# Performance work log

Measured on AMD Instinct MI355X. Metric: run time of the kernel, lower is better.

The kernel has to match this reference:

```python
import jax, jax.numpy as jnp
import numpy as np

L = 4       # num_fourier_layers
W = 256     # width
NF = 256    # num_freq (no_low_freq)
B = 2       # batch size
N = 16384   # num_nodes per graph
E = 524288  # total edges (avg degree 16)
D_IN = 3    # darcy input features


def lin(x, w, b):
    # torch nn.Linear convention: w is (out, in)
    return x @ w.T + b


def layernorm(x, s, b):
    m = x.mean(-1, keepdims=True)
    v = x.var(-1, keepdims=True)
    return (x - m) / jnp.sqrt(v + 1e-5) * s + b


def setup_inputs() -> dict:
    key = jax.random.key(0)
    ks = jax.random.split(key, 16)
    s = lambda i, shape, sc=0.05: sc * jax.random.normal(ks[i], shape, jnp.float32)
    inp = {
        "x": jax.random.normal(ks[0], (B * N, D_IN), jnp.float32),
        "U": jax.random.normal(ks[1], (B, N, NF), jnp.float32) / np.float32(np.sqrt(N)),
        "edge_index": jax.random.randint(ks[2], (2, E), 0, B * N),
        "edge_weight": jax.random.uniform(ks[3], (E,), jnp.float32),
        "lif_embed": jax.random.normal(ks[4], (B * N, 16), jnp.float32),
        "p_w": s(5, (W, D_IN)), "p_b": jnp.zeros((W,), jnp.float32),
        # scale = 1/(in*out) * rand, per GraphFourierLayer
        "four_w": (1.0 / (W * W)) * jax.random.uniform(ks[6], (L, W, W, NF), jnp.float32),
        "w_w": s(7, (L, W, W)), "w_b": jnp.zeros((L, W), jnp.float32),
        "ln_s": jnp.ones((L, W), jnp.float32), "ln_b": jnp.zeros((L, W), jnp.float32),
        "lin_w": s(8, (L, W, W)), "lin_b": jnp.zeros((L, W), jnp.float32),
        "ew_w": s(9, (L, 16, 1)), "ew_b": jnp.zeros((L, 16), jnp.float32),
        "g1_w": s(10, (L, 3, 48)), "g1_b": jnp.zeros((L, 3), jnp.float32),
        "g2_w": s(11, (L, 1, 3)), "g2_b": jnp.zeros((L, 1), jnp.float32),
        "proj_w": s(12, (W, 2 * W)), "proj_b": jnp.zeros((W,), jnp.float32),
        "q1_w": s(13, (128, W)), "q1_b": jnp.zeros((128,), jnp.float32),
        "q2_w": s(14, (1, 128)), "q2_b": jnp.zeros((1,), jnp.float32),
    }
    return inp


def reference(x, U, edge_index, edge_weight, lif_embed,
              p_w, p_b, four_w, w_w, w_b, ln_s, ln_b,
              lin_w, lin_b, ew_w, ew_b, g1_w, g1_b, g2_w, g2_b,
              proj_w, proj_b, q1_w, q1_b, q2_w, q2_b):
    src = edge_index[0]  # edge_index_j (source)
    dst = edge_index[1]  # edge_index_i (target, aggr='add')
    h = lin(x, p_w, p_b)  # [B*N, W]

    for l in range(L):
        # --- GraphFourierLayer: batched spectral transform ---
        h3 = h.reshape(B, N, W)
        x_ft = jnp.einsum('bnf,bnw->bfw', U, h3)          # U^T x  -> [B, NF, W]
        out_ft = jnp.einsum('bfi,iof->bfo', x_ft, four_w[l])
        x1 = jnp.einsum('bnf,bfw->bnw', U, out_ft).reshape(B * N, W)
        xf = jax.nn.gelu(x1 + lin(h, w_w[l], w_b[l]), approximate=False)
        xf = layernorm(xf, ln_s[l], ln_b[l])

        # --- FrigateConv: gather -> edge MLP gate -> scatter-add -> L2 normalize ---
        xs = lin(h, lin_w[l], lin_b[l])
        ew = lin(edge_weight[:, None], ew_w[l], ew_b[l])  # [E, 16]
        gin = jnp.concatenate([ew, lif_embed[dst], lif_embed[src]], axis=1)  # [E, 48]
        g = jax.nn.sigmoid(lin(jax.nn.relu(lin(gin, g1_w[l], g1_b[l])), g2_w[l], g2_b[l]))
        msg = xs[src] * g                                  # [E, W]
        agg = jax.ops.segment_sum(msg, dst, num_segments=B * N)
        nrm = jnp.maximum(jnp.linalg.norm(agg, axis=-1, keepdims=True), 1e-12)
        xs = agg / nrm

        h = lin(jnp.concatenate([xf, xs], axis=1), proj_w, proj_b)

    out = lin(jax.nn.relu(lin(h, q1_w, q1_b)), q2_w, q2_b)  # q: MLP(W,1,128)
    return out
```

## Files before the change

### kernel.cpp

```cpp
#include <hip/hip_runtime.h>
#include <hip/hip_bf16.h>

#define B_ 2
#define N_ 16384
#define BN 32768
#define W_ 256
#define NF_ 256
#define E_ 524288
#define L_ 4
#define KS_ 32

typedef __attribute__((ext_vector_type(8))) short bf16x8;
typedef __attribute__((ext_vector_type(4))) float f32x4;

__device__ __forceinline__ unsigned short f2b(float x) {
    __hip_bfloat16 h = __float2bfloat16(x);
    return *reinterpret_cast<unsigned short*>(&h);
}
__device__ __forceinline__ float b2f(unsigned short u) {
    union { unsigned int i; float f; } c; c.i = ((unsigned int)u) << 16; return c.f;
}
__device__ __forceinline__ float geluf(float x) {
    return 0.5f * x * (1.0f + erff(x * 0.70710678118654752440f));
}

template<bool DUAL, int OUTM, bool BIAS>
__global__ __launch_bounds__(256) void k_mfma_nt(
    const unsigned short* __restrict__ A1, int lda1, long A1o, long A1i,
    const unsigned short* __restrict__ B1, int ldb1, long B1o, long B1i, int K1,
    const unsigned short* __restrict__ A2, int lda2, long A2o,
    const unsigned short* __restrict__ B2, int ldb2, long B2o, int K2,
    void* __restrict__ Cv, int ldc, long Co, long Ci,
    const float* __restrict__ bias, int zdiv)
{
    __shared__ unsigned short lds[16384];
    const int t = threadIdx.x;
    const int wid = t >> 6, lane = t & 63;
    const int wr = wid >> 1, wc = wid & 1;
    const int m0 = blockIdx.y * 128, n0 = blockIdx.x * 128;
    const int z = blockIdx.z;
    const int zo = z / zdiv, zi = z - zo * zdiv;
    A1 += zo * A1o + zi * A1i;
    B1 += zo * B1o + zi * B1i;
    if (DUAL) { A2 += zo * A2o; B2 += zo * B2o; }

    const int srow  = t >> 3;
    const int sgran = (t & 7) ^ (srow & 7);
    const int rlo   = lane & 15;
    const int hi    = lane >> 4;

    f32x4 acc[4][4] = {};

    const int nph = DUAL ? 2 : 1;
    for (int ph = 0; ph < nph; ++ph) {
        const unsigned short* A  = (DUAL && ph) ? A2 : A1;
        const unsigned short* Bp = (DUAL && ph) ? B2 : B1;
        const int lda = (DUAL && ph) ? lda2 : lda1;
        const int ldb = (DUAL && ph) ? ldb2 : ldb1;
        const int K   = (DUAL && ph) ? K2 : K1;
        for (int k0 = 0; k0 < K; k0 += 64) {
            __syncthreads();
            #pragma unroll
            for (int j = 0; j < 4; ++j) {
                const unsigned short* ga = A + (long)(m0 + j*32 + srow) * lda + k0 + sgran*8;
                __builtin_amdgcn_global_load_lds(
                    (const __attribute__((address_space(1))) void*)ga,
                    (__attribute__((address_space(3))) void*)&lds[(j*4 + wid) * 512],
                    16, 0, 0);
            }
            #pragma unroll
            for (int j = 0; j < 4; ++j) {
                const unsigned short* gb = Bp + (long)(n0 + j*32 + srow) * ldb + k0 + sgran*8;
                __builtin_amdgcn_global_load_lds(
                    (const __attribute__((address_space(1))) void*)gb,
                    (__attribute__((address_space(3))) void*)&lds[8192 + (j*4 + wid) * 512],
                    16, 0, 0);
            }
            __syncthreads();
            #pragma unroll
            for (int kk = 0; kk < 2; ++kk) {
                const int g8 = (((kk*4 + hi) ^ (lane & 7)) << 3);
                bf16x8 a[4], b[4];
                #pragma unroll
                for (int fm = 0; fm < 4; ++fm)
                    a[fm] = *(const bf16x8*)&lds[(wr*64 + fm*16 + rlo)*64 + g8];
                #pragma unroll
                for (int fn = 0; fn < 4; ++fn)
                    b[fn] = *(const bf16x8*)&lds[8192 + (wc*64 + fn*16 + rlo)*64 + g8];
                #pragma unroll
                for (int fm = 0; fm < 4; ++fm)
                    #pragma unroll
                    for (int fn = 0; fn < 4; ++fn)
                        acc[fm][fn] = __builtin_amdgcn_mfma_f32_16x16x32_bf16(
                            a[fm], b[fn], acc[fm][fn], 0, 0, 0);
            }
        }
    }

    const int mb = m0 + wr*64, nb = n0 + wc*64;
    if (OUTM == 1) {
        unsigned short* C = (unsigned short*)Cv + zo * Co + zi * Ci;
        #pragma unroll
        for (int fn = 0; fn < 4; ++fn) {
            const int n = nb + fn*16 + rlo;
            const float bv = BIAS ? bias[n] : 0.f;
            #pragma unroll
            for (int fm = 0; fm < 4; ++fm)
                #pragma unroll
                for (int r = 0; r < 4; ++r) {
                    const int m = mb + fm*16 + hi*4 + r;
                    C[(long)m*ldc + n] = f2b(acc[fm][fn][r] + bv);
                }
        }
    } else {
        float* C = (float*)Cv + zo * Co + zi * Ci;
        #pragma unroll
        for (int fn = 0; fn < 4; ++fn) {
            const int n = nb + fn*16 + rlo;
            const float bv = BIAS ? bias[n] : 0.f;
            #pragma unroll
            for (int fm = 0; fm < 4; ++fm)
                #pragma unroll
                for (int r = 0; r < 4; ++r) {
                    const int m = mb + fm*16 + hi*4 + r;
                    C[(long)m*ldc + n] = acc[fm][fn][r] + bv;
                }
        }
    }
}

__global__ __launch_bounds__(256) void k_cvt(const float* __restrict__ s, unsigned short* __restrict__ d) {
    long i = (long)(blockIdx.x * 256 + threadIdx.x) * 4;
    float4 v = *(const float4*)&s[i];
    ushort4 u = {f2b(v.x), f2b(v.y), f2b(v.z), f2b(v.w)};
    *(ushort4*)&d[i] = u;
}

__global__ __launch_bounds__(256) void k_cvtT(
    const float* __restrict__ src, unsigned short* __restrict__ dT, unsigned short* __restrict__ dL)
{
    const int b = blockIdx.z;
    src += (long)b * N_ * NF_; dT += (long)b * N_ * NF_; dL += (long)b * N_ * NF_;
    const int r0 = blockIdx.y * 64, c0 = blockIdx.x * 64;
    __shared__ unsigned short tile[64][72];
    const int t = threadIdx.x, lr = t >> 4, lc4 = (t & 15) * 4;
    #pragma unroll
    for (int p = 0; p < 4; ++p) {
        int r = p*16 + lr;
        float4 v = *(const float4*)&src[(long)(r0+r)*NF_ + c0 + lc4];
        ushort4 u = {f2b(v.x), f2b(v.y), f2b(v.z), f2b(v.w)};
        *(ushort4*)&dL[(long)(r0+r)*NF_ + c0 + lc4] = u;
        tile[r][lc4+0]=u.x; tile[r][lc4+1]=u.y; tile[r][lc4+2]=u.z; tile[r][lc4+3]=u.w;
    }
    __syncthreads();
    #pragma unroll
    for (int p = 0; p < 4; ++p) {
        int c = p*16 + lr;
        ushort4 u = {tile[lc4+0][c], tile[lc4+1][c], tile[lc4+2][c], tile[lc4+3][c]};
        *(ushort4*)&dT[(long)(c0+c)*N_ + r0 + lc4] = u;
    }
}

__global__ __launch_bounds__(256) void k_T_b2b(
    const unsigned short* __restrict__ src, unsigned short* __restrict__ dst)
{
    const int b = blockIdx.z;
    src += (long)b * N_ * W_; dst += (long)b * N_ * W_;
    const int r0 = blockIdx.y * 64, c0 = blockIdx.x * 64;
    __shared__ unsigned short tile[64][72];
    const int t = threadIdx.x, lr = t >> 4, lc4 = (t & 15) * 4;
    #pragma unroll
    for (int p = 0; p < 4; ++p) {
        int r = p*16 + lr;
        ushort4 v = *(const ushort4*)&src[(long)(r0+r)*W_ + c0 + lc4];
        tile[r][lc4+0]=v.x; tile[r][lc4+1]=v.y; tile[r][lc4+2]=v.z; tile[r][lc4+3]=v.w;
    }
    __syncthreads();
    #pragma unroll
    for (int p = 0; p < 4; ++p) {
        int c = p*16 + lr;
        ushort4 u = {tile[lc4+0][c], tile[lc4+1][c], tile[lc4+2][c], tile[lc4+3][c]};
        *(ushort4*)&dst[(long)(c0+c)*N_ + r0 + lc4] = u;
    }
}

__global__ __launch_bounds__(256) void k_in_proj(
    const float* __restrict__ x, const float* __restrict__ pw,
    const float* __restrict__ pb, unsigned short* __restrict__ h)
{
    int idx = blockIdx.x * 256 + threadIdx.x;
    int node = idx >> 8, w = idx & 255;
    float x0 = x[node*3+0], x1 = x[node*3+1], x2 = x[node*3+2];
    h[idx] = f2b(fmaf(x0, pw[w*3+0], fmaf(x1, pw[w*3+1], fmaf(x2, pw[w*3+2], pb[w]))));
}

__global__ __launch_bounds__(256) void k_reduce_ks(
    const float* __restrict__ part, float* __restrict__ outp)
{
    int idx = blockIdx.x * 256 + threadIdx.x;
    int b = idx >> 16, rem = idx & 65535;
    const float* p = part + (long)b * KS_ * 65536 + rem;
    float s = 0.f;
    #pragma unroll
    for (int k = 0; k < KS_; ++k) s += p[(long)k * 65536];
    outp[idx] = s;
}

__global__ __launch_bounds__(256) void k_fourier_mul(
    const float* __restrict__ fw, const float* __restrict__ xftT,
    unsigned short* __restrict__ oftT)
{
    const int o = blockIdx.x, f = threadIdx.x;
    const float* fwp = fw + (long)o * NF_ + f;
    float a0 = 0.f, a1 = 0.f;
    #pragma unroll 8
    for (int i = 0; i < W_; ++i) {
        float w = fwp[(long)i * W_ * NF_];
        a0 = fmaf(xftT[i*NF_ + f], w, a0);
        a1 = fmaf(xftT[65536 + i*NF_ + f], w, a1);
    }
    oftT[o*NF_ + f] = f2b(a0);
    oftT[65536 + o*NF_ + f] = f2b(a1);
}

__global__ __launch_bounds__(256) void k_gelu_ln(
    const float* __restrict__ xf, unsigned short* __restrict__ out,
    const float* __restrict__ wb, const float* __restrict__ lns, const float* __restrict__ lnb)
{
    const int node = blockIdx.x * 4 + (threadIdx.x >> 6);
    const int lane = threadIdx.x & 63;
    float4 v = *(const float4*)(xf + (long)node*W_ + lane*4);
    float4 bb = *(const float4*)(wb + lane*4);
    float e0 = geluf(v.x+bb.x), e1 = geluf(v.y+bb.y);
    float e2 = geluf(v.z+bb.z), e3 = geluf(v.w+bb.w);
    float s  = e0+e1+e2+e3;
    float s2 = e0*e0+e1*e1+e2*e2+e3*e3;
    #pragma unroll
    for (int o = 32; o; o >>= 1) { s += __shfl_xor(s, o); s2 += __shfl_xor(s2, o); }
    float mean = s * (1.0f/W_);
    float var  = s2 * (1.0f/W_) - mean*mean;
    float inv = rsqrtf(var + 1e-5f);
    float4 sc = *(const float4*)(lns + lane*4);
    float4 bi = *(const float4*)(lnb + lane*4);
    ushort4 o4;
    o4.x = f2b((e0-mean)*inv*sc.x + bi.x);
    o4.y = f2b((e1-mean)*inv*sc.y + bi.y);
    o4.z = f2b((e2-mean)*inv*sc.z + bi.z);
    o4.w = f2b((e3-mean)*inv*sc.w + bi.w);
    *(ushort4*)(out + (long)node*W_ + lane*4) = o4;
}

__global__ __launch_bounds__(256) void k_hist(const int* __restrict__ ei, int* __restrict__ count) {
    int e = blockIdx.x * 256 + threadIdx.x;
    atomicAdd(&count[ei[E_ + e]], 1);
}
__global__ __launch_bounds__(256) void k_scan(const int* __restrict__ count, int* __restrict__ offsets) {
    __shared__ int sums[256];
    const int t = threadIdx.x;
    const int base = t * 128;
    int s = 0;
    for (int i = 0; i < 128; ++i) s += count[base + i];
    sums[t] = s;
    __syncthreads();
    for (int off = 1; off < 256; off <<= 1) {
        int v = (t >= off) ? sums[t - off] : 0;
        __syncthreads();
        sums[t] += v;
        __syncthreads();
    }
    int run = (t == 0) ? 0 : sums[t - 1];
    for (int i = 0; i < 128; ++i) { offsets[base + i] = run; run += count[base + i]; }
    if (t == 255) offsets[BN] = run;
}
__global__ __launch_bounds__(256) void k_place(
    const int* __restrict__ ei, const float* __restrict__ ewt,
    const int* __restrict__ offsets, int* __restrict__ cursor,
    int* __restrict__ srcp, float* __restrict__ ewt_p)
{
    int e = blockIdx.x * 256 + threadIdx.x;
    int dst = ei[E_ + e];
    int pos = offsets[dst] + atomicAdd(&cursor[dst], 1);
    srcp[pos] = ei[e];
    ewt_p[pos] = ewt[e];
}

__global__ __launch_bounds__(256) void k_gate_agg(
    const int* __restrict__ offsets, const int* __restrict__ srcp,
    const float* __restrict__ ewt_p, const float* __restrict__ lif,
    const float* __restrict__ eww, const float* __restrict__ ewb,
    const float* __restrict__ g1w, const float* __restrict__ g1b,
    const float* __restrict__ g2w, const float* __restrict__ g2b,
    const unsigned short* __restrict__ xs, unsigned short* __restrict__ out)
{
    const int node = blockIdx.x * 4 + (threadIdx.x >> 6);
    const int lane = threadIdx.x & 63;
    const int beg = offsets[node], end = offsets[node + 1];
    float lifd[16];
    #pragma unroll
    for (int j = 0; j < 16; ++j) lifd[j] = lif[node*16 + j];
    float a0=0.f, a1=0.f, a2=0.f, a3=0.f;
    for (int c0 = beg; c0 < end; c0 += 64) {
        const int p = c0 + lane;
        float gate = 0.f; int src = 0;
        if (p < end) {
            src = srcp[p];
            const float wv = ewt_p[p];
            float t0 = g1b[0], t1 = g1b[1], t2 = g1b[2];
            #pragma unroll
            for (int j = 0; j < 16; ++j) {
                const float e0 = fmaf(wv, eww[j], ewb[j]);
                const float l1 = lifd[j];
                const float l2 = lif[src*16 + j];
                t0 = fmaf(g1w[j], e0, t0);
                t0 = fmaf(g1w[16 + j], l1, t0);
                t0 = fmaf(g1w[32 + j], l2, t0);
                t1 = fmaf(g1w[48 + j], e0, t1);
                t1 = fmaf(g1w[64 + j], l1, t1);
                t1 = fmaf(g1w[80 + j], l2, t1);
                t2 = fmaf(g1w[96 + j], e0, t2);
                t2 = fmaf(g1w[112 + j], l1, t2);
                t2 = fmaf(g1w[128 + j], l2, t2);
            }
            float z = g2b[0];
            z = fmaf(g2w[0], fmaxf(t0, 0.f), z);
            z = fmaf(g2w[1], fmaxf(t1, 0.f), z);
            z = fmaf(g2w[2], fmaxf(t2, 0.f), z);
            gate = 1.f / (1.f + __expf(-z));
        }
        const int m = min(64, end - c0);
        for (int j = 0; j < m; ++j) {
            const float gv = __shfl(gate, j);
            const int   s  = __shfl(src, j);
            ushort4 v = *(const ushort4*)&xs[(long)s * W_ + lane * 4];
            a0 = fmaf(b2f(v.x), gv, a0);
            a1 = fmaf(b2f(v.y), gv, a1);
            a2 = fmaf(b2f(v.z), gv, a2);
            a3 = fmaf(b2f(v.w), gv, a3);
        }
    }
    float s = a0*a0 + a1*a1 + a2*a2 + a3*a3;
    #pragma unroll
    for (int o = 32; o; o >>= 1) s += __shfl_xor(s, o);
    float inv = 1.f / fmaxf(sqrtf(s), 1e-12f);
    ushort4 r = {f2b(a0*inv), f2b(a1*inv), f2b(a2*inv), f2b(a3*inv)};
    *(ushort4*)(out + (long)node * W_ + lane * 4) = r;
}

__global__ __launch_bounds__(256) void k_q2(
    const float* __restrict__ q1o, const float* __restrict__ q2w,
    const float* __restrict__ q2b, float* __restrict__ out)
{
    int node = blockIdx.x * 4 + (threadIdx.x >> 6);
    int lane = threadIdx.x & 63;
    float a = fmaxf(q1o[(long)node*128 + lane], 0.f) * q2w[lane]
            + fmaxf(q1o[(long)node*128 + 64 + lane], 0.f) * q2w[64 + lane];
    #pragma unroll
    for (int o = 32; o; o >>= 1) a += __shfl_xor(a, o);
    if (lane == 0) out[node] = a + q2b[0];
}

extern "C" void kernel_launch(void* const* d_in, const int* in_sizes, int n_in,
                              void* d_out, int out_size, void* d_ws, size_t ws_size,
                              hipStream_t stream)
{
    const float* x      = (const float*)d_in[0];
    const float* U      = (const float*)d_in[1];
    const int*   ei     = (const int*)  d_in[2];
    const float* ewt    = (const float*)d_in[3];
    const float* lif    = (const float*)d_in[4];
    const float* p_w    = (const float*)d_in[5];
    const float* p_b    = (const float*)d_in[6];
    const float* four_w = (const float*)d_in[7];
    const float* w_w    = (const float*)d_in[8];
    const float* w_b    = (const float*)d_in[9];
    const float* ln_s   = (const float*)d_in[10];
    const float* ln_b   = (const float*)d_in[11];
    const float* lin_w  = (const float*)d_in[12];
    const float* lin_b  = (const float*)d_in[13];
    const float* ew_w   = (const float*)d_in[14];
    const float* ew_b   = (const float*)d_in[15];
    const float* g1_w   = (const float*)d_in[16];
    const float* g1_b   = (const float*)d_in[17];
    const float* g2_w   = (const float*)d_in[18];
    const float* g2_b   = (const float*)d_in[19];
    const float* proj_w = (const float*)d_in[20];
    const float* proj_b = (const float*)d_in[21];
    const float* q1_w   = (const float*)d_in[22];
    const float* q1_b   = (const float*)d_in[23];
    const float* q2_w   = (const float*)d_in[24];
    const float* q2_b   = (const float*)d_in[25];

    char* wsb = (char*)d_ws;
    size_t off = 0;
    auto alloc = [&](size_t bytes) -> void* {
        void* p = wsb + off; off += (bytes + 255) & ~(size_t)255; return p;
    };
    float* xf        = (float*)alloc((size_t)BN * W_ * 4);
    float* xft_part  = (float*)alloc((size_t)B_ * KS_ * 65536 * 4);
    float* xftT      = (float*)alloc((size_t)B_ * 65536 * 4);
    unsigned short* h_bf   = (unsigned short*)alloc((size_t)BN * W_ * 2);
    unsigned short* hT_bf  = (unsigned short*)alloc((size_t)BN * W_ * 2);
    unsigned short* U_bf   = (unsigned short*)alloc((size_t)BN * NF_ * 2);
    unsigned short* UT_bf  = (unsigned short*)alloc((size_t)BN * NF_ * 2);
    unsigned short* xf_bf  = (unsigned short*)alloc((size_t)BN * W_ * 2);
    unsigned short* xs_bf  = (unsigned short*)alloc((size_t)BN * W_ * 2);
    unsigned short* xsn_bf = (unsigned short*)alloc((size_t)BN * W_ * 2);
    unsigned short* oftT_bf= (unsigned short*)alloc((size_t)B_ * 65536 * 2);
    unsigned short* wwb    = (unsigned short*)alloc((size_t)L_ * W_ * W_ * 2);
    unsigned short* linwb  = (unsigned short*)alloc((size_t)L_ * W_ * W_ * 2);
    unsigned short* projwb = (unsigned short*)alloc((size_t)W_ * 2 * W_ * 2);
    unsigned short* q1wb   = (unsigned short*)alloc((size_t)128 * W_ * 2);
    int*   srcp    = (int*)alloc((size_t)E_ * 4);
    float* ewt_p   = (float*)alloc((size_t)E_ * 4);
    int*   count   = (int*)alloc((size_t)BN * 4);
    int*   cursor  = (int*)alloc((size_t)BN * 4);
    int*   offsets = (int*)alloc((size_t)(BN + 1) * 4);

    hipMemsetAsync(count, 0, (size_t)2 * BN * 4, stream);
    k_hist<<<E_/256, 256, 0, stream>>>(ei, count);
    k_scan<<<1, 256, 0, stream>>>(count, offsets);
    k_place<<<E_/256, 256, 0, stream>>>(ei, ewt, offsets, cursor, srcp, ewt_p);

    k_cvt<<<(L_*W_*W_)/1024, 256, 0, stream>>>(w_w, wwb);
    k_cvt<<<(L_*W_*W_)/1024, 256, 0, stream>>>(lin_w, linwb);
    k_cvt<<<(W_*2*W_)/1024, 256, 0, stream>>>(proj_w, projwb);
    k_cvt<<<(128*W_)/1024, 256, 0, stream>>>(q1_w, q1wb);
    k_cvtT<<<dim3(NF_/64, N_/64, B_), 256, 0, stream>>>(U, UT_bf, U_bf);

    k_in_proj<<<BN, 256, 0, stream>>>(x, p_w, p_b, h_bf);

    for (int l = 0; l < L_; ++l) {
        k_T_b2b<<<dim3(W_/64, N_/64, B_), 256, 0, stream>>>(h_bf, hT_bf);
        k_mfma_nt<false,0,false><<<dim3(2, 2, B_*KS_), 256, 0, stream>>>(
            hT_bf, N_, (long)W_*N_, N_/KS_,
            UT_bf, N_, (long)NF_*N_, N_/KS_, N_/KS_,
            nullptr, 0, 0, nullptr, 0, 0, 0,
            xft_part, NF_, (long)KS_*65536, 65536,
            nullptr, KS_);
        k_reduce_ks<<<(B_*65536)/256, 256, 0, stream>>>(xft_part, xftT);
        k_fourier_mul<<<W_, 256, 0, stream>>>(four_w + (long)l*W_*W_*NF_, xftT, oftT_bf);
        k_mfma_nt<true,0,false><<<dim3(2, N_/128, B_), 256, 0, stream>>>(
            U_bf, NF_, (long)N_*NF_, 0,
            oftT_bf, NF_, (long)65536, 0, NF_,
            h_bf, W_, (long)N_*W_,
            wwb + (long)l*W_*W_, W_, 0, W_,
            xf, W_, (long)N_*W_, 0,
            nullptr, 1);
        k_gelu_ln<<<BN/4, 256, 0, stream>>>(xf, xf_bf, w_b + l*W_, ln_s + l*W_, ln_b + l*W_);
        k_mfma_nt<false,1,true><<<dim3(2, BN/128, 1), 256, 0, stream>>>(
            h_bf, W_, 0, 0,
            linwb + (long)l*W_*W_, W_, 0, 0, W_,
            nullptr, 0, 0, nullptr, 0, 0, 0,
            xs_bf, W_, 0, 0,
            lin_b + l*W_, 1);
        k_gate_agg<<<BN/4, 256, 0, stream>>>(offsets, srcp, ewt_p, lif,
            ew_w + l*16, ew_b + l*16, g1_w + l*144, g1_b + l*3,
            g2_w + l*3, g2_b + l, xs_bf, xsn_bf);
        k_mfma_nt<true,1,true><<<dim3(2, BN/128, 1), 256, 0, stream>>>(
            xf_bf, W_, 0, 0,
            projwb, 2*W_, 0, 0, W_,
            xsn_bf, W_, 0,
            projwb + W_, 2*W_, 0, W_,
            h_bf, W_, 0, 0,
            proj_b, 1);
    }
    k_mfma_nt<false,0,true><<<dim3(1, BN/128, 1), 256, 0, stream>>>(
        h_bf, W_, 0, 0,
        q1wb, W_, 0, 0, W_,
        nullptr, 0, 0, nullptr, 0, 0, 0,
        xf, 128, 0, 0,
        q1_b, 1);
    k_q2<<<BN/4, 256, 0, stream>>>(xf, q2_w, q2_b, (float*)d_out);
}
```

Measured before the change: 846.6 us.

## Precompute all-layer edge gates once and fuse h transpose into projection GEMM

The edge gate MLP depends only on edge weights and lif embeddings, so all four layers' gates are now computed in one upfront kernel and stored per layer. This lets the per-layer aggregation kernel just read gates, dropping the per-layer gate computation and the shuffle-based chunking. Separately, the projection GEMM epilogue now also writes a transposed copy of h, which removes the per-layer standalone transpose kernel at the cost of strided 8-byte stores and an extra 8 MB gate buffer.

After: 888.1 us. 1.05x slower.

```diff
diff --git a/kernel.cpp b/kernel.cpp
--- a/kernel.cpp
+++ b/kernel.cpp
@@ -24,13 +24,14 @@
     return 0.5f * x * (1.0f + erff(x * 0.70710678118654752440f));
 }
 
-template<bool DUAL, int OUTM, bool BIAS>
+template<bool DUAL, int OUTM, bool BIAS, bool TROUT = false>
 __global__ __launch_bounds__(256) void k_mfma_nt(
     const unsigned short* __restrict__ A1, int lda1, long A1o, long A1i,
     const unsigned short* __restrict__ B1, int ldb1, long B1o, long B1i, int K1,
     const unsigned short* __restrict__ A2, int lda2, long A2o,
     const unsigned short* __restrict__ B2, int ldb2, long B2o, int K2,
     void* __restrict__ Cv, int ldc, long Co, long Ci,
+    unsigned short* __restrict__ CT,
     const float* __restrict__ bias, int zdiv)
 {
     __shared__ unsigned short lds[16384];
@@ -105,12 +106,20 @@
             const int n = nb + fn*16 + rlo;
             const float bv = BIAS ? bias[n] : 0.f;
             #pragma unroll
-            for (int fm = 0; fm < 4; ++fm)
+            for (int fm = 0; fm < 4; ++fm) {
+                unsigned short vals[4];
                 #pragma unroll
                 for (int r = 0; r < 4; ++r) {
                     const int m = mb + fm*16 + hi*4 + r;
-                    C[(long)m*ldc + n] = f2b(acc[fm][fn][r] + bv);
+                    vals[r] = f2b(acc[fm][fn][r] + bv);
+                    C[(long)m*ldc + n] = vals[r];
                 }
+                if (TROUT) {
+                    const int m_base = mb + fm*16 + hi*4;
+                    const int b = m_base >> 14, loc = m_base & 16383;
+                    *(ushort4*)&CT[((long)b*ldc + n)*N_ + loc] = *(ushort4*)vals;
+                }
+            }
         }
     } else {
         float* C = (float*)Cv + zo * Co + zi * Ci;
@@ -284,13 +293,13 @@
     ewt_p[pos] = ewt[e];
 }
 
-__global__ __launch_bounds__(256) void k_gate_agg(
+__global__ __launch_bounds__(256) void k_gate4(
     const int* __restrict__ offsets, const int* __restrict__ srcp,
     const float* __restrict__ ewt_p, const float* __restrict__ lif,
-    const float* __restrict__ eww, const float* __restrict__ ewb,
-    const float* __restrict__ g1w, const float* __restrict__ g1b,
-    const float* __restrict__ g2w, const float* __restrict__ g2b,
-    const unsigned short* __restrict__ xs, unsigned short* __restrict__ out)
+    const float* __restrict__ ew_w, const float* __restrict__ ew_b,
+    const float* __restrict__ g1_w, const float* __restrict__ g1_b,
+    const float* __restrict__ g2_w, const float* __restrict__ g2_b,
+    float* __restrict__ gp)
 {
     const int node = blockIdx.x * 4 + (threadIdx.x >> 6);
     const int lane = threadIdx.x & 63;
@@ -298,45 +307,58 @@
     float lifd[16];
     #pragma unroll
     for (int j = 0; j < 16; ++j) lifd[j] = lif[node*16 + j];
-    float a0=0.f, a1=0.f, a2=0.f, a3=0.f;
-    for (int c0 = beg; c0 < end; c0 += 64) {
-        const int p = c0 + lane;
-        float gate = 0.f; int src = 0;
-        if (p < end) {
-            src = srcp[p];
-            const float wv = ewt_p[p];
+    for (int p = beg + lane; p < end; p += 64) {
+        const int src = srcp[p];
+        const float wv = ewt_p[p];
+        float lifs[16];
+        #pragma unroll
+        for (int j = 0; j < 16; ++j) lifs[j] = lif[src*16 + j];
+        for (int l = 0; l < L_; ++l) {
+            const float* eww = ew_w + l*16;
+            const float* ewb = ew_b + l*16;
+            const float* g1w = g1_w + l*144;
+            const float* g1b = g1_b + l*3;
+            const float* g2w = g2_w + l*3;
             float t0 = g1b[0], t1 = g1b[1], t2 = g1b[2];
             #pragma unroll
             for (int j = 0; j < 16; ++j) {
                 const float e0 = fmaf(wv, eww[j], ewb[j]);
-                const float l1 = lifd[j];
-                const float l2 = lif[src*16 + j];
                 t0 = fmaf(g1w[j], e0, t0);
-                t0 = fmaf(g1w[16 + j], l1, t0);
-                t0 = fmaf(g1w[32 + j], l2, t0);
+                t0 = fmaf(g1w[16 + j], lifd[j], t0);
+                t0 = fmaf(g1w[32 + j], lifs[j], t0);
                 t1 = fmaf(g1w[48 + j], e0, t1);
-                t1 = fmaf(g1w[64 + j], l1, t1);
-                t1 = fmaf(g1w[80 + j], l2, t1);
+                t1 = fmaf(g1w[64 + j], lifd[j], t1);
+                t1 = fmaf(g1w[80 + j], lifs[j], t1);
                 t2 = fmaf(g1w[96 + j], e0, t2);
-                t2 = fmaf(g1w[112 + j], l1, t2);
-                t2 = fmaf(g1w[128 + j], l2, t2);
+                t2 = fmaf(g1w[112 + j], lifd[j], t2);
+                t2 = fmaf(g1w[128 + j], lifs[j], t2);
             }
-            float z = g2b[0];
+            float z = g2_b[l];
             z = fmaf(g2w[0], fmaxf(t0, 0.f), z);
             z = fmaf(g2w[1], fmaxf(t1, 0.f), z);
             z = fmaf(g2w[2], fmaxf(t2, 0.f), z);
-            gate = 1.f / (1.f + __expf(-z));
+            gp[(long)l*E_ + p] = 1.f / (1.f + __expf(-z));
         }
-        const int m = min(64, end - c0);
-        for (int j = 0; j < m; ++j) {
-            const float gv = __shfl(gate, j);
-            const int   s  = __shfl(src, j);
-            ushort4 v = *(const ushort4*)&xs[(long)s * W_ + lane * 4];
-            a0 = fmaf(b2f(v.x), gv, a0);
-            a1 = fmaf(b2f(v.y), gv, a1);
-            a2 = fmaf(b2f(v.z), gv, a2);
-            a3 = fmaf(b2f(v.w), gv, a3);
-        }
+    }
+}
+
+__global__ __launch_bounds__(256) void k_agg_norm(
+    const int* __restrict__ offsets, const int* __restrict__ srcp,
+    const float* __restrict__ gp, const unsigned short* __restrict__ xs,
+    unsigned short* __restrict__ out)
+{
+    const int node = blockIdx.x * 4 + (threadIdx.x >> 6);
+    const int lane = threadIdx.x & 63;
+    const int beg = offsets[node], end = offsets[node + 1];
+    float a0=0.f, a1=0.f, a2=0.f, a3=0.f;
+    for (int p = beg; p < end; ++p) {
+        const int src = srcp[p];
+        const float gv = gp[p];
+        ushort4 v = *(const ushort4*)&xs[(long)src * W_ + lane * 4];
+        a0 = fmaf(b2f(v.x), gv, a0);
+        a1 = fmaf(b2f(v.y), gv, a1);
+        a2 = fmaf(b2f(v.z), gv, a2);
+        a3 = fmaf(b2f(v.w), gv, a3);
     }
     float s = a0*a0 + a1*a1 + a2*a2 + a3*a3;
     #pragma unroll
@@ -398,6 +420,7 @@
     float* xf        = (float*)alloc((size_t)BN * W_ * 4);
     float* xft_part  = (float*)alloc((size_t)B_ * KS_ * 65536 * 4);
     float* xftT      = (float*)alloc((size_t)B_ * 65536 * 4);
+    float* gp        = (float*)alloc((size_t)L_ * E_ * 4);
     unsigned short* h_bf   = (unsigned short*)alloc((size_t)BN * W_ * 2);
     unsigned short* hT_bf  = (unsigned short*)alloc((size_t)BN * W_ * 2);
     unsigned short* U_bf   = (unsigned short*)alloc((size_t)BN * NF_ * 2);
@@ -420,6 +443,8 @@
     k_hist<<<E_/256, 256, 0, stream>>>(ei, count);
     k_scan<<<1, 256, 0, stream>>>(count, offsets);
     k_place<<<E_/256, 256, 0, stream>>>(ei, ewt, offsets, cursor, srcp, ewt_p);
+    k_gate4<<<BN/4, 256, 0, stream>>>(offsets, srcp, ewt_p, lif,
+        ew_w, ew_b, g1_w, g1_b, g2_w, g2_b, gp);
 
     k_cvt<<<(L_*W_*W_)/1024, 256, 0, stream>>>(w_w, wwb);
     k_cvt<<<(L_*W_*W_)/1024, 256, 0, stream>>>(lin_w, linwb);
@@ -428,15 +453,15 @@
     k_cvtT<<<dim3(NF_/64, N_/64, B_), 256, 0, stream>>>(U, UT_bf, U_bf);
 
     k_in_proj<<<BN, 256, 0, stream>>>(x, p_w, p_b, h_bf);
+    k_T_b2b<<<dim3(W_/64, N_/64, B_), 256, 0, stream>>>(h_bf, hT_bf);
 
     for (int l = 0; l < L_; ++l) {
-        k_T_b2b<<<dim3(W_/64, N_/64, B_), 256, 0, stream>>>(h_bf, hT_bf);
         k_mfma_nt<false,0,false><<<dim3(2, 2, B_*KS_), 256, 0, stream>>>(
             hT_bf, N_, (long)W_*N_, N_/KS_,
             UT_bf, N_, (long)NF_*N_, N_/KS_, N_/KS_,
             nullptr, 0, 0, nullptr, 0, 0, 0,
             xft_part, NF_, (long)KS_*65536, 65536,
-            nullptr, KS_);
+            nullptr, nullptr, KS_);
         k_reduce_ks<<<(B_*65536)/256, 256, 0, stream>>>(xft_part, xftT);
         k_fourier_mul<<<W_, 256, 0, stream>>>(four_w + (long)l*W_*W_*NF_, xftT, oftT_bf);
         k_mfma_nt<true,0,false><<<dim3(2, N_/128, B_), 256, 0, stream>>>(
@@ -445,30 +470,28 @@
             h_bf, W_, (long)N_*W_,
             wwb + (long)l*W_*W_, W_, 0, W_,
             xf, W_, (long)N_*W_, 0,
-            nullptr, 1);
+            nullptr, nullptr, 1);
         k_gelu_ln<<<BN/4, 256, 0, stream>>>(xf, xf_bf, w_b + l*W_, ln_s + l*W_, ln_b + l*W_);
         k_mfma_nt<false,1,true><<<dim3(2, BN/128, 1), 256, 0, stream>>>(
             h_bf, W_, 0, 0,
             linwb + (long)l*W_*W_, W_, 0, 0, W_,
             nullptr, 0, 0, nullptr, 0, 0, 0,
             xs_bf, W_, 0, 0,
-            lin_b + l*W_, 1);
-        k_gate_agg<<<BN/4, 256, 0, stream>>>(offsets, srcp, ewt_p, lif,
-            ew_w + l*16, ew_b + l*16, g1_w + l*144, g1_b + l*3,
-            g2_w + l*3, g2_b + l, xs_bf, xsn_bf);
-        k_mfma_nt<true,1,true><<<dim3(2, BN/128, 1), 256, 0, stream>>>(
+            nullptr, lin_b + l*W_, 1);
+        k_agg_norm<<<BN/4, 256, 0, stream>>>(offsets, srcp, gp + (long)l*E_, xs_bf, xsn_bf);
+        k_mfma_nt<true,1,true,true><<<dim3(2, BN/128, 1), 256, 0, stream>>>(
             xf_bf, W_, 0, 0,
             projwb, 2*W_, 0, 0, W_,
             xsn_bf, W_, 0,
             projwb + W_, 2*W_, 0, W_,
             h_bf, W_, 0, 0,
-            proj_b, 1);
+            hT_bf, proj_b, 1);
     }
     k_mfma_nt<false,0,true><<<dim3(1, BN/128, 1), 256, 0, stream>>>(
         h_bf, W_, 0, 0,
         q1wb, W_, 0, 0, W_,
         nullptr, 0, 0, nullptr, 0, 0, 0,
         xf, 128, 0, 0,
-        q1_b, 1);
+        nullptr, q1_b, 1);
     k_q2<<<BN/4, 256, 0, stream>>>(xf, q2_w, q2_b, (float*)d_out);
 }
```
